# Optimization experiments

Measured on AMD Instinct MI355X. Metric: run time of the kernel, lower is better.

## Reference

```python
import jax, jax.numpy as jnp
import numpy as np

B, N_LR, N_HR, D, NH, L, K = 16, 256, 512, 512, 8, 4, 4
FF = 4 * D

def _ln(x, g, b):
    m = jnp.mean(x, -1, keepdims=True)
    v = jnp.var(x, -1, keepdims=True)
    return (x - m) * jax.lax.rsqrt(v + 1e-5) * g + b

def _gelu(x):
    return jax.nn.gelu(x, approximate=False)  # torch nn.GELU default = exact

def _attn(x, qkvW, qkvb, projW, projb, bias):
    b, n, d = x.shape
    hd = d // NH
    qkv = (x @ qkvW + qkvb).reshape(b, n, 3, NH, hd).transpose(2, 0, 3, 1, 4)
    q, k, v = qkv[0], qkv[1], qkv[2]
    a = jnp.einsum('bhnd,bhmd->bhnm', q, k) * (hd ** -0.5)
    if bias is not None:
        a = a + bias
    a = jax.nn.softmax(a, axis=-1)
    o = jnp.einsum('bhnm,bhmd->bhnd', a, v).transpose(0, 2, 1, 3).reshape(b, n, d)
    return o @ projW + projb

def _ffn(x, W1, b1, W2, b2):
    return _gelu(x @ W1 + b1) @ W2 + b2

def setup_inputs() -> dict:
    key = jax.random.key(0)
    ks = iter(jax.random.split(key, 64))
    def rn(shape, s=0.02):
        return jax.random.normal(next(ks), shape, jnp.float32) * s
    inp = {}
    A = rn((B, N_LR, N_LR), 1.0)
    A = 0.5 * (A + A.transpose(0, 2, 1))  # symmetric weighted adjacency
    inp['A_lr'] = A
    inp['X_lr'] = A  # node features = adjacency rows, as in the original model
    inp['ip_W'] = rn((N_LR, D)); inp['ip_b'] = jnp.zeros(D)
    inp['ip_g'] = jnp.ones(D); inp['ip_bt'] = jnp.zeros(D)
    inp['e_n1g'] = jnp.ones((L, D)); inp['e_n1b'] = jnp.zeros((L, D))
    inp['e_qkvW'] = rn((L, D, 3 * D)); inp['e_qkvb'] = jnp.zeros((L, 3 * D))
    inp['e_projW'] = rn((L, D, D)); inp['e_projb'] = jnp.zeros((L, D))
    inp['e_ebW'] = rn((L, NH), 1.0); inp['e_ebs'] = jnp.full((L,), 0.1)
    inp['e_n2g'] = jnp.ones((L, D)); inp['e_n2b'] = jnp.zeros((L, D))
    inp['e_f1W'] = rn((L, D, FF)); inp['e_f1b'] = jnp.zeros((L, FF))
    inp['e_f2W'] = rn((L, FF, D)); inp['e_f2b'] = jnp.zeros((L, D))
    inp['encn_g'] = jnp.ones(D); inp['encn_b'] = jnp.zeros(D)
    inp['up1W'] = rn((N_LR, N_HR)); inp['up1b'] = jnp.zeros(N_HR)
    inp['up2W'] = rn((N_HR, N_HR)); inp['up2b'] = jnp.zeros(N_HR)
    inp['r_n1g'] = jnp.ones(D); inp['r_n1b'] = jnp.zeros(D)
    inp['r_qkvW'] = rn((D, 3 * D)); inp['r_qkvb'] = jnp.zeros(3 * D)
    inp['r_projW'] = rn((D, D)); inp['r_projb'] = jnp.zeros(D)
    inp['r_n2g'] = jnp.ones(D); inp['r_n2b'] = jnp.zeros(D)
    inp['r_f1W'] = rn((D, FF)); inp['r_f1b'] = jnp.zeros(FF)
    inp['r_f2W'] = rn((FF, D)); inp['r_f2b'] = jnp.zeros(D)
    inp['hrn_g'] = jnp.ones(D); inp['hrn_b'] = jnp.zeros(D)
    inp['dec_W'] = rn((K, D, D)); inp['dec_b'] = jnp.full((1,), 3.0)
    return inp

def reference(A_lr, X_lr, ip_W, ip_b, ip_g, ip_bt, e_n1g, e_n1b, e_qkvW, e_qkvb, e_projW, e_projb, e_ebW, e_ebs, e_n2g, e_n2b, e_f1W, e_f1b, e_f2W, e_f2b, encn_g, encn_b, up1W, up1b, up2W, up2b, r_n1g, r_n1b, r_qkvW, r_qkvb, r_projW, r_projb, r_n2g, r_n2b, r_f1W, r_f1b, r_f2W, r_f2b, hrn_g, hrn_b, dec_W, dec_b):
    # input_proj: Linear -> LayerNorm -> GELU (dropout is identity in eval)
    H = _gelu(_ln(X_lr @ ip_W + ip_b, ip_g, ip_bt))  # (B, n_lr, D)
    # encoder: pre-norm blocks with additive per-head edge bias in softmax
    for l in range(L):
        bias = e_ebs[l] * A_lr[:, None, :, :] * e_ebW[l][None, :, None, None]  # (B,NH,N,N)
        H = H + _attn(_ln(H, e_n1g[l], e_n1b[l]), e_qkvW[l], e_qkvb[l], e_projW[l], e_projb[l], bias)
        H = H + _ffn(_ln(H, e_n2g[l], e_n2b[l]), e_f1W[l], e_f1b[l], e_f2W[l], e_f2b[l])
    H = _ln(H, encn_g, encn_b)
    # upsample n_lr -> n_hr along node axis (applied on transposed H)
    Ht = H.transpose(0, 2, 1)                      # (B, D, n_lr)
    Ht = _gelu(Ht @ up1W + up1b) @ up2W + up2b     # (B, D, n_hr)
    H = Ht.transpose(0, 2, 1)                      # (B, n_hr, D)
    # HR refinement: standard pre-norm self-attention block
    H = H + _attn(_ln(H, r_n1g, r_n1b), r_qkvW, r_qkvb, r_projW, r_projb, None)
    H = H + _ffn(_ln(H, r_n2g, r_n2b), r_f1W, r_f1b, r_f2W, r_f2b)
    H = _ln(H, hrn_g, hrn_b)
    # bilinear multi-head decoder: mean_k H W_k H^T, symmetrized
    A_pred = jnp.einsum('bnd,kde,bme->bnm', H, dec_W, H) / K
    A_pred = 0.5 * (A_pred + A_pred.transpose(0, 2, 1))
    iu, ju = np.triu_indices(N_HR, k=1)
    pred = A_pred[:, iu, ju]                        # (B, n_hr*(n_hr-1)/2)
    return jax.nn.softplus(pred + dec_b[0])
```

## Files before the change

### kernel.cpp

```cpp
#include <hip/hip_runtime.h>
#include <hip/hip_bf16.h>
#include <math.h>

#define DEV __device__ __forceinline__

typedef __attribute__((ext_vector_type(8))) short bf16x8;
typedef __attribute__((ext_vector_type(4))) float f32x4;

DEV float gelu_f(float x) { return 0.5f * x * (1.0f + erff(x * 0.70710678118654752f)); }

DEV float block_reduce(float v, bool is_sum, float* red) {
#pragma unroll
  for (int off = 32; off > 0; off >>= 1) {
    float o = __shfl_down(v, off, 64);
    v = is_sum ? (v + o) : fmaxf(v, o);
  }
  __syncthreads();
  if ((threadIdx.x & 63) == 0) red[threadIdx.x >> 6] = v;
  __syncthreads();
  return is_sum ? (red[0] + red[1] + red[2] + red[3])
                : fmaxf(fmaxf(red[0], red[1]), fmaxf(red[2], red[3]));
}

DEV short bf16s(float x) {
  __hip_bfloat16 v = __float2bfloat16(x);
  return *reinterpret_cast<short*>(&v);
}

DEV void async16(void* lds, const void* g) {
  __builtin_amdgcn_global_load_lds(
      (const __attribute__((address_space(1))) unsigned int*)g,
      (__attribute__((address_space(3))) unsigned int*)lds, 16, 0, 0);
}

__global__ __launch_bounds__(256) void conv_kernel(
    const float* __restrict__ X, __hip_bfloat16* __restrict__ Y, int n) {
  int i = blockIdx.x * 256 + threadIdx.x;
  if (i < n) Y[i] = __float2bfloat16(X[i]);
}

__global__ __launch_bounds__(256) void tconv_kernel(
    const float* __restrict__ X, __hip_bfloat16* __restrict__ Y, int R, int C) {
  __shared__ float t[32][33];
  const float* xb = X + (size_t)blockIdx.z * R * C;
  __hip_bfloat16* yb = Y + (size_t)blockIdx.z * R * C;
  int c0 = blockIdx.x * 32, r0 = blockIdx.y * 32;
  int tx = threadIdx.x & 31, ty = threadIdx.x >> 5;
  for (int i = ty; i < 32; i += 8) t[i][tx] = xb[(size_t)(r0 + i) * C + c0 + tx];
  __syncthreads();
  for (int i = ty; i < 32; i += 8)
    yb[(size_t)(c0 + i) * R + r0 + tx] = __float2bfloat16(t[tx][i]);
}

__global__ __launch_bounds__(256) void build_s_kernel(
    const float* __restrict__ W, __hip_bfloat16* __restrict__ S, int D, int Kk) {
  int i = blockIdx.x * 256 + threadIdx.x;
  if (i >= D * D) return;
  int d = i / D, e = i % D;
  float s = 0.f;
  for (int k = 0; k < Kk; ++k) {
    s += W[(size_t)k * D * D + i];
    s += W[(size_t)k * D * D + (size_t)e * D + d];
  }
  S[i] = __float2bfloat16(s / (2.0f * Kk));
}

__global__ __launch_bounds__(256) void mgemm_kernel(
    const __hip_bfloat16* __restrict__ A, const __hip_bfloat16* __restrict__ Bt,
    const float* __restrict__ bias, const float* __restrict__ resid,
    float* __restrict__ outf, __hip_bfloat16* __restrict__ outb,
    int M, int N, int K, int act, int mgrp) {
  __shared__ __align__(16) short As[64 * 64];
  __shared__ __align__(16) short Bs[64 * 64];
  const int tid = threadIdx.x;
  const int lane = tid & 63, wave = tid >> 6;
  const int quad = lane >> 4, l15 = lane & 15;
  const int bid = blockIdx.x;
  const int g = bid & 7, sidx = bid >> 3;
  const int mt = g * mgrp + sidx % mgrp;
  const int nt = sidx / mgrp;
  const int row0 = mt * 64, col0 = nt * 64;
  const short* Ag = (const short*)A;
  const short* Bg = (const short*)Bt;
  f32x4 acc[4] = {};

  for (int k0 = 0; k0 < K; k0 += 64) {
    __syncthreads();
#pragma unroll
    for (int i = 0; i < 2; ++i) {
      int c = (wave * 2 + i) * 64 + lane;
      int r = c >> 3, pp = c & 7;
      int kc = pp ^ (r & 7);
      async16(&As[(wave * 2 + i) * 512], &Ag[(size_t)(row0 + r) * K + k0 + kc * 8]);
      async16(&Bs[(wave * 2 + i) * 512], &Bg[(size_t)(col0 + r) * K + k0 + kc * 8]);
    }
    __syncthreads();
#pragma unroll
    for (int kh = 0; kh < 2; ++kh) {
      const int ch = ((quad + kh * 4) ^ (l15 & 7)) * 8;
      bf16x8 af = *(const bf16x8*)&As[(wave * 16 + l15) * 64 + ch];
#pragma unroll
      for (int ni = 0; ni < 4; ++ni) {
        bf16x8 bq = *(const bf16x8*)&Bs[(ni * 16 + l15) * 64 + ch];
        acc[ni] = __builtin_amdgcn_mfma_f32_16x16x32_bf16(af, bq, acc[ni], 0, 0, 0);
      }
    }
  }

#pragma unroll
  for (int ni = 0; ni < 4; ++ni) {
    int cc = col0 + ni * 16 + l15;
    float bb = bias ? bias[cc] : 0.f;
#pragma unroll
    for (int r = 0; r < 4; ++r) {
      int rr = row0 + wave * 16 + quad * 4 + r;
      size_t idx = (size_t)rr * N + cc;
      float v = acc[ni][r] + bb;
      if (act) v = gelu_f(v);
      if (resid) v += resid[idx];
      if (outf) outf[idx] = v;
      if (outb) outb[idx] = __float2bfloat16(v);
    }
  }
}

__global__ __launch_bounds__(256) void qkv_gemm_kernel(
    const __hip_bfloat16* __restrict__ A, const __hip_bfloat16* __restrict__ Bt,
    const float* __restrict__ bias, __hip_bfloat16* __restrict__ qkv,
    int M, int K, int nseq, int lgn, int mgrp) {
  __shared__ __align__(16) short As[64 * 64];
  __shared__ __align__(16) short Bs[64 * 64];
  const int tid = threadIdx.x;
  const int lane = tid & 63, wave = tid >> 6;
  const int quad = lane >> 4, l15 = lane & 15;
  const int bid = blockIdx.x;
  const int g = bid & 7, sidx = bid >> 3;
  const int mt = g * mgrp + sidx % mgrp;
  const int nt = sidx / mgrp;
  const int row0 = mt * 64, col0 = nt * 64;
  const short* Ag = (const short*)A;
  const short* Bg = (const short*)Bt;
  f32x4 acc[4] = {};

  for (int k0 = 0; k0 < K; k0 += 64) {
    __syncthreads();
#pragma unroll
    for (int i = 0; i < 2; ++i) {
      int c = (wave * 2 + i) * 64 + lane;
      int r = c >> 3, pp = c & 7;
      int kc = pp ^ (r & 7);
      async16(&As[(wave * 2 + i) * 512], &Ag[(size_t)(row0 + r) * K + k0 + kc * 8]);
      async16(&Bs[(wave * 2 + i) * 512], &Bg[(size_t)(col0 + r) * K + k0 + kc * 8]);
    }
    __syncthreads();
#pragma unroll
    for (int kh = 0; kh < 2; ++kh) {
      const int ch = ((quad + kh * 4) ^ (l15 & 7)) * 8;
      bf16x8 af = *(const bf16x8*)&As[(wave * 16 + l15) * 64 + ch];
#pragma unroll
      for (int ni = 0; ni < 4; ++ni) {
        bf16x8 bq = *(const bf16x8*)&Bs[(ni * 16 + l15) * 64 + ch];
        acc[ni] = __builtin_amdgcn_mfma_f32_16x16x32_bf16(af, bq, acc[ni], 0, 0, 0);
      }
    }
  }

  const size_t PART = (size_t)M * 512;
#pragma unroll
  for (int ni = 0; ni < 4; ++ni) {
    int cc = col0 + ni * 16 + l15;
    float bb = bias ? bias[cc] : 0.f;
    int which = cc >> 9;
    int h = (cc >> 6) & 7;
    int d = cc & 63;
#pragma unroll
    for (int r = 0; r < 4; ++r) {
      int rr = row0 + wave * 16 + quad * 4 + r;
      int b = rr >> lgn;
      int nn = rr & (nseq - 1);
      float v = acc[ni][r] + bb;
      size_t dst;
      if (which == 2) {
        dst = 2 * PART + (((size_t)b * 8 + h) * 64 + d) * nseq + nn;
      } else {
        dst = (size_t)which * PART + (((size_t)b * 8 + h) * nseq + nn) * 64 + d;
      }
      qkv[dst] = __float2bfloat16(v);
    }
  }
}

__global__ __launch_bounds__(256) void fattn_kernel(
    const __hip_bfloat16* __restrict__ Qh, const __hip_bfloat16* __restrict__ Kh,
    const __hip_bfloat16* __restrict__ Vt, __hip_bfloat16* __restrict__ O,
    const float* __restrict__ Abias, const float* __restrict__ ebW,
    const float* __restrict__ ebs, int N) {
  __shared__ __align__(16) short Ks[64][72];
  __shared__ __align__(16) short Vs[64][72];
  __shared__ __align__(16) short Ps[4][16][72];
  const int qt = blockIdx.x, h = blockIdx.y, b = blockIdx.z;
  const int tid = threadIdx.x, lane = tid & 63, wave = tid >> 6;
  const int quad = lane >> 4, l15 = lane & 15;
  const size_t hb = (size_t)b * 8 + h;
  const short* Qg = (const short*)Qh + hb * N * 64;
  const short* Kg = (const short*)Kh + hb * N * 64;
  const short* Vg = (const short*)Vt + hb * 64 * N;
  const float scale = 0.125f;
  const bool hasb = (Abias != nullptr);
  const float bscale = hasb ? ebs[0] * ebW[h] : 0.f;
  const int qrow_w = qt * 64 + wave * 16;

  bf16x8 qf0 = *(const bf16x8*)&Qg[(size_t)(qrow_w + l15) * 64 + quad * 8];
  bf16x8 qf1 = *(const bf16x8*)&Qg[(size_t)(qrow_w + l15) * 64 + quad * 8 + 32];

  float m_i[4], l_i[4];
  f32x4 oacc[4] = {};
#pragma unroll
  for (int r = 0; r < 4; ++r) { m_i[r] = -1e30f; l_i[r] = 0.f; }

  for (int k0 = 0; k0 < N; k0 += 64) {
    __syncthreads();
#pragma unroll
    for (int i = 0; i < 2; ++i) {
      int idx = i * 256 + tid;
      int r = idx >> 3, ch = idx & 7;
      *(uint4*)&Ks[r][ch * 8] = *(const uint4*)&Kg[(size_t)(k0 + r) * 64 + ch * 8];
      *(uint4*)&Vs[r][ch * 8] = *(const uint4*)&Vg[(size_t)r * N + k0 + ch * 8];
    }
    __syncthreads();

    f32x4 s[4] = {};
#pragma unroll
    for (int ni = 0; ni < 4; ++ni) {
      bf16x8 kf0 = *(const bf16x8*)&Ks[ni * 16 + l15][quad * 8];
      bf16x8 kf1 = *(const bf16x8*)&Ks[ni * 16 + l15][quad * 8 + 32];
      s[ni] = __builtin_amdgcn_mfma_f32_16x16x32_bf16(qf0, kf0, s[ni], 0, 0, 0);
      s[ni] = __builtin_amdgcn_mfma_f32_16x16x32_bf16(qf1, kf1, s[ni], 0, 0, 0);
    }
    if (hasb) {
#pragma unroll
      for (int ni = 0; ni < 4; ++ni)
#pragma unroll
        for (int r = 0; r < 4; ++r) {
          int qq = qrow_w + quad * 4 + r;
          int kk = k0 + ni * 16 + l15;
          s[ni][r] = s[ni][r] * scale + bscale * Abias[((size_t)b * N + qq) * N + kk];
        }
    } else {
#pragma unroll
      for (int ni = 0; ni < 4; ++ni)
#pragma unroll
        for (int r = 0; r < 4; ++r) s[ni][r] *= scale;
    }

    float mt[4];
#pragma unroll
    for (int r = 0; r < 4; ++r)
      mt[r] = fmaxf(fmaxf(s[0][r], s[1][r]), fmaxf(s[2][r], s[3][r]));
#pragma unroll
    for (int off = 1; off < 16; off <<= 1)
#pragma unroll
      for (int r = 0; r < 4; ++r) mt[r] = fmaxf(mt[r], __shfl_xor(mt[r], off, 64));

    float alpha[4];
#pragma unroll
    for (int r = 0; r < 4; ++r) {
      float mn = fmaxf(m_i[r], mt[r]);
      alpha[r] = __expf(m_i[r] - mn);
      m_i[r] = mn;
    }
    float ls[4] = {0.f, 0.f, 0.f, 0.f};
#pragma unroll
    for (int ni = 0; ni < 4; ++ni)
#pragma unroll
      for (int r = 0; r < 4; ++r) {
        float p = __expf(s[ni][r] - m_i[r]);
        s[ni][r] = p;
        ls[r] += p;
      }
#pragma unroll
    for (int off = 1; off < 16; off <<= 1)
#pragma unroll
      for (int r = 0; r < 4; ++r) ls[r] += __shfl_xor(ls[r], off, 64);
#pragma unroll
    for (int r = 0; r < 4; ++r) l_i[r] = l_i[r] * alpha[r] + ls[r];
#pragma unroll
    for (int ni = 0; ni < 4; ++ni)
#pragma unroll
      for (int r = 0; r < 4; ++r) oacc[ni][r] *= alpha[r];

#pragma unroll
    for (int ni = 0; ni < 4; ++ni)
#pragma unroll
      for (int r = 0; r < 4; ++r)
        Ps[wave][quad * 4 + r][ni * 16 + l15] = bf16s(s[ni][r]);

    bf16x8 pf0 = *(const bf16x8*)&Ps[wave][l15][quad * 8];
    bf16x8 pf1 = *(const bf16x8*)&Ps[wave][l15][quad * 8 + 32];
#pragma unroll
    for (int ni = 0; ni < 4; ++ni) {
      bf16x8 vf0 = *(const bf16x8*)&Vs[ni * 16 + l15][quad * 8];
      bf16x8 vf1 = *(const bf16x8*)&Vs[ni * 16 + l15][quad * 8 + 32];
      oacc[ni] = __builtin_amdgcn_mfma_f32_16x16x32_bf16(pf0, vf0, oacc[ni], 0, 0, 0);
      oacc[ni] = __builtin_amdgcn_mfma_f32_16x16x32_bf16(pf1, vf1, oacc[ni], 0, 0, 0);
    }
  }

  float inv[4];
#pragma unroll
  for (int r = 0; r < 4; ++r) inv[r] = 1.f / l_i[r];
#pragma unroll
  for (int ni = 0; ni < 4; ++ni)
#pragma unroll
    for (int r = 0; r < 4; ++r) {
      int nn = qrow_w + quad * 4 + r;
      int col = h * 64 + ni * 16 + l15;
      O[((size_t)b * N + nn) * 512 + col] = __float2bfloat16(oacc[ni][r] * inv[r]);
    }
}

__global__ __launch_bounds__(256) void dec_mfma_kernel(
    const __hip_bfloat16* __restrict__ Tb_, const __hip_bfloat16* __restrict__ Hb_,
    const float* __restrict__ dec_b, float* __restrict__ out) {
  const int Nn = 512, K = 512;
  __shared__ __align__(16) short As[64 * 64];
  __shared__ __align__(16) short Bs[64 * 64];
  int p = blockIdx.x;
  int bb = blockIdx.y;
  int it = 0, rem = p;
  while (rem >= 8 - it) { rem -= 8 - it; ++it; }
  int jt = it + rem;
  const int row0 = it * 64, col0 = jt * 64;
  const int tid = threadIdx.x;
  const int lane = tid & 63, wave = tid >> 6;
  const int quad = lane >> 4, l15 = lane & 15;
  const int wr = (wave >> 1) * 32, wc = (wave & 1) * 32;
  const short* Ag = (const short*)(Tb_ + (size_t)bb * Nn * K);
  const short* Bg = (const short*)(Hb_ + (size_t)bb * Nn * K);
  f32x4 acc[2][2] = {};

  for (int k0 = 0; k0 < K; k0 += 64) {
    __syncthreads();
#pragma unroll
    for (int i = 0; i < 2; ++i) {
      int c = (wave * 2 + i) * 64 + lane;
      int r = c >> 3, pp = c & 7;
      int kc = pp ^ (r & 7);
      async16(&As[(wave * 2 + i) * 512], &Ag[(size_t)(row0 + r) * K + k0 + kc * 8]);
      async16(&Bs[(wave * 2 + i) * 512], &Bg[(size_t)(col0 + r) * K + k0 + kc * 8]);
    }
    __syncthreads();
#pragma unroll
    for (int kh = 0; kh < 2; ++kh) {
      const int ch = ((quad + kh * 4) ^ (l15 & 7)) * 8;
      bf16x8 af[2], bq[2];
#pragma unroll
      for (int mi = 0; mi < 2; ++mi)
        af[mi] = *(const bf16x8*)&As[(wr + mi * 16 + l15) * 64 + ch];
#pragma unroll
      for (int ni = 0; ni < 2; ++ni)
        bq[ni] = *(const bf16x8*)&Bs[(wc + ni * 16 + l15) * 64 + ch];
#pragma unroll
      for (int mi = 0; mi < 2; ++mi)
#pragma unroll
        for (int ni = 0; ni < 2; ++ni)
          acc[mi][ni] = __builtin_amdgcn_mfma_f32_16x16x32_bf16(af[mi], bq[ni], acc[mi][ni], 0, 0, 0);
    }
  }

  float db = dec_b[0];
  size_t obase = (size_t)bb * ((size_t)Nn * (Nn - 1) / 2);
#pragma unroll
  for (int mi = 0; mi < 2; ++mi) {
#pragma unroll
    for (int ni = 0; ni < 2; ++ni) {
      int j = col0 + wc + ni * 16 + l15;
#pragma unroll
      for (int r = 0; r < 4; ++r) {
        int i = row0 + wr + mi * 16 + quad * 4 + r;
        if (j > i) {
          float x = acc[mi][ni][r] + db;
          float sp = fmaxf(x, 0.f) + __logf(1.f + __expf(-fabsf(x)));
          out[obase + (size_t)i * (2 * Nn - i - 1) / 2 + (j - i - 1)] = sp;
        }
      }
    }
  }
}

__global__ __launch_bounds__(256) void ln_kernel(
    const float* __restrict__ X, float* __restrict__ outf,
    __hip_bfloat16* __restrict__ outb, const float* __restrict__ g,
    const float* __restrict__ b, int D, int do_gelu) {
  __shared__ float red[4];
  int row = blockIdx.x;
  const float* x = X + (size_t)row * D;
  float s = 0.f, s2 = 0.f;
  for (int d = threadIdx.x; d < D; d += 256) {
    float v = x[d];
    s += v;
    s2 += v * v;
  }
  s = block_reduce(s, true, red);
  s2 = block_reduce(s2, true, red);
  float mean = s / D;
  float var = s2 / D - mean * mean;
  float inv = rsqrtf(var + 1e-5f);
  for (int d = threadIdx.x; d < D; d += 256) {
    float v = (x[d] - mean) * inv * g[d] + b[d];
    if (do_gelu) v = gelu_f(v);
    if (outf) outf[(size_t)row * D + d] = v;
    if (outb) outb[(size_t)row * D + d] = __float2bfloat16(v);
  }
}

template <typename T>
__global__ __launch_bounds__(256) void transpose_kernel(
    const T* __restrict__ X, T* __restrict__ Y, int R, int C) {
  __shared__ T t[32][33];
  const T* xb = X + (size_t)blockIdx.z * R * C;
  T* yb = Y + (size_t)blockIdx.z * R * C;
  int c0 = blockIdx.x * 32, r0 = blockIdx.y * 32;
  int tx = threadIdx.x & 31, ty = threadIdx.x >> 5;
  for (int i = ty; i < 32; i += 8) t[i][tx] = xb[(size_t)(r0 + i) * C + c0 + tx];
  __syncthreads();
  for (int i = ty; i < 32; i += 8) yb[(size_t)(c0 + i) * R + r0 + tx] = t[tx][i];
}

extern "C" void kernel_launch(void* const* d_in, const int* in_sizes, int n_in,
                              void* d_out, int out_size, void* d_ws, size_t ws_size,
                              hipStream_t stream) {
  const float *A_lr = (const float*)d_in[0], *X_lr = (const float*)d_in[1],
              *ip_W = (const float*)d_in[2], *ip_b = (const float*)d_in[3],
              *ip_g = (const float*)d_in[4], *ip_bt = (const float*)d_in[5],
              *e_n1g = (const float*)d_in[6], *e_n1b = (const float*)d_in[7],
              *e_qkvW = (const float*)d_in[8], *e_qkvb = (const float*)d_in[9],
              *e_projW = (const float*)d_in[10], *e_projb = (const float*)d_in[11],
              *e_ebW = (const float*)d_in[12], *e_ebs = (const float*)d_in[13],
              *e_n2g = (const float*)d_in[14], *e_n2b = (const float*)d_in[15],
              *e_f1W = (const float*)d_in[16], *e_f1b = (const float*)d_in[17],
              *e_f2W = (const float*)d_in[18], *e_f2b = (const float*)d_in[19],
              *encn_g = (const float*)d_in[20], *encn_b = (const float*)d_in[21],
              *up1W = (const float*)d_in[22], *up1b = (const float*)d_in[23],
              *up2W = (const float*)d_in[24], *up2b = (const float*)d_in[25],
              *r_n1g = (const float*)d_in[26], *r_n1b = (const float*)d_in[27],
              *r_qkvW = (const float*)d_in[28], *r_qkvb = (const float*)d_in[29],
              *r_projW = (const float*)d_in[30], *r_projb = (const float*)d_in[31],
              *r_n2g = (const float*)d_in[32], *r_n2b = (const float*)d_in[33],
              *r_f1W = (const float*)d_in[34], *r_f1b = (const float*)d_in[35],
              *r_f2W = (const float*)d_in[36], *r_f2b = (const float*)d_in[37],
              *hrn_g = (const float*)d_in[38], *hrn_b = (const float*)d_in[39],
              *dec_W = (const float*)d_in[40], *dec_b = (const float*)d_in[41];

  const int Bb = 16, NLR = 256, NHR = 512, Dm = 512, NHh = 8, FF = 2048, Ll = 4;
  typedef __hip_bfloat16 bf;

  float* ws = (float*)d_ws;
  float* H = ws;
  float* Hf = ws + 4194304;
  bf* XNb = (bf*)(ws + 8388608);
  bf* AOb = (bf*)(ws + 10485760);
  bf* BIGb = (bf*)(ws + 12582912);
  bf* WB = (bf*)(ws + 20971520);
  bf* Xlrb = (bf*)(ws + 29229056);

  size_t o = 0;
  bf* ipWt = WB + o;   o += (size_t)512 * 256;
  bf* eqkvT = WB + o;  o += (size_t)4 * 1536 * 512;
  bf* eprojT = WB + o; o += (size_t)4 * 512 * 512;
  bf* ef1T = WB + o;   o += (size_t)4 * 2048 * 512;
  bf* ef2T = WB + o;   o += (size_t)4 * 512 * 2048;
  bf* up1T = WB + o;   o += (size_t)512 * 256;
  bf* up2T = WB + o;   o += (size_t)512 * 512;
  bf* rqkvT = WB + o;  o += (size_t)1536 * 512;
  bf* rprojT = WB + o; o += (size_t)512 * 512;
  bf* rf1T = WB + o;   o += (size_t)2048 * 512;
  bf* rf2T = WB + o;   o += (size_t)512 * 2048;
  bf* Sb = WB + o;     o += (size_t)512 * 512;

  bf* Q_e = BIGb;
  bf* K_e = BIGb + 2097152;
  bf* V_e = BIGb + 4194304;
  bf* Q_r = BIGb;
  bf* K_r = BIGb + 4194304;
  bf* V_r = BIGb + 8388608;

  tconv_kernel<<<dim3(16, 8, 1), 256, 0, stream>>>(ip_W, ipWt, 256, 512);
  tconv_kernel<<<dim3(48, 16, 4), 256, 0, stream>>>(e_qkvW, eqkvT, 512, 1536);
  tconv_kernel<<<dim3(16, 16, 4), 256, 0, stream>>>(e_projW, eprojT, 512, 512);
  tconv_kernel<<<dim3(64, 16, 4), 256, 0, stream>>>(e_f1W, ef1T, 512, 2048);
  tconv_kernel<<<dim3(16, 64, 4), 256, 0, stream>>>(e_f2W, ef2T, 2048, 512);
  tconv_kernel<<<dim3(16, 8, 1), 256, 0, stream>>>(up1W, up1T, 256, 512);
  tconv_kernel<<<dim3(16, 16, 1), 256, 0, stream>>>(up2W, up2T, 512, 512);
  tconv_kernel<<<dim3(48, 16, 1), 256, 0, stream>>>(r_qkvW, rqkvT, 512, 1536);
  tconv_kernel<<<dim3(16, 16, 1), 256, 0, stream>>>(r_projW, rprojT, 512, 512);
  tconv_kernel<<<dim3(64, 16, 1), 256, 0, stream>>>(r_f1W, rf1T, 512, 2048);
  tconv_kernel<<<dim3(16, 64, 1), 256, 0, stream>>>(r_f2W, rf2T, 2048, 512);
  conv_kernel<<<(1048576 + 255) / 256, 256, 0, stream>>>(X_lr, Xlrb, 1048576);
  build_s_kernel<<<(512 * 512 + 255) / 256, 256, 0, stream>>>(dec_W, Sb, Dm, 4);

  mgemm_kernel<<<64 * 8, 256, 0, stream>>>(
      Xlrb, ipWt, ip_b, nullptr, Hf, nullptr, Bb * NLR, Dm, NLR, 0, 8);
  ln_kernel<<<Bb * NLR, 256, 0, stream>>>(Hf, H, nullptr, ip_g, ip_bt, Dm, 1);

  for (int l = 0; l < Ll; ++l) {
    ln_kernel<<<Bb * NLR, 256, 0, stream>>>(H, nullptr, XNb, e_n1g + l * Dm, e_n1b + l * Dm, Dm, 0);
    qkv_gemm_kernel<<<64 * 24, 256, 0, stream>>>(
        XNb, eqkvT + (size_t)l * 1536 * 512, e_qkvb + l * 1536, BIGb,
        Bb * NLR, Dm, NLR, 8, 8);
    fattn_kernel<<<dim3(4, 8, 16), 256, 0, stream>>>(
        Q_e, K_e, V_e, AOb, A_lr, e_ebW + l * NHh, e_ebs + l, NLR);
    mgemm_kernel<<<64 * 8, 256, 0, stream>>>(
        AOb, eprojT + (size_t)l * 512 * 512, e_projb + l * Dm, H,
        H, nullptr, Bb * NLR, Dm, Dm, 0, 8);
    ln_kernel<<<Bb * NLR, 256, 0, stream>>>(H, nullptr, XNb, e_n2g + l * Dm, e_n2b + l * Dm, Dm, 0);
    mgemm_kernel<<<64 * 32, 256, 0, stream>>>(
        XNb, ef1T + (size_t)l * 2048 * 512, e_f1b + l * FF, nullptr,
        nullptr, BIGb, Bb * NLR, FF, Dm, 1, 8);
    mgemm_kernel<<<64 * 8, 256, 0, stream>>>(
        BIGb, ef2T + (size_t)l * 512 * 2048, e_f2b + l * Dm, H,
        H, nullptr, Bb * NLR, Dm, FF, 0, 8);
  }

  ln_kernel<<<Bb * NLR, 256, 0, stream>>>(H, nullptr, XNb, encn_g, encn_b, Dm, 0);
  transpose_kernel<bf><<<dim3(16, 8, Bb), 256, 0, stream>>>(XNb, AOb, NLR, Dm);
  mgemm_kernel<<<128 * 8, 256, 0, stream>>>(
      AOb, up1T, up1b, nullptr, nullptr, BIGb, Bb * Dm, NHR, NLR, 1, 16);
  mgemm_kernel<<<128 * 8, 256, 0, stream>>>(
      BIGb, up2T, up2b, nullptr, Hf, nullptr, Bb * Dm, NHR, NHR, 0, 16);
  transpose_kernel<float><<<dim3(16, 16, Bb), 256, 0, stream>>>(Hf, H, Dm, NHR);

  ln_kernel<<<Bb * NHR, 256, 0, stream>>>(H, nullptr, XNb, r_n1g, r_n1b, Dm, 0);
  qkv_gemm_kernel<<<128 * 24, 256, 0, stream>>>(
      XNb, rqkvT, r_qkvb, BIGb, Bb * NHR, Dm, NHR, 9, 16);
  fattn_kernel<<<dim3(8, 8, 16), 256, 0, stream>>>(
      Q_r, K_r, V_r, AOb, nullptr, nullptr, nullptr, NHR);
  mgemm_kernel<<<128 * 8, 256, 0, stream>>>(
      AOb, rprojT, r_projb, H, H, nullptr, Bb * NHR, Dm, Dm, 0, 16);
  ln_kernel<<<Bb * NHR, 256, 0, stream>>>(H, nullptr, XNb, r_n2g, r_n2b, Dm, 0);
  mgemm_kernel<<<128 * 32, 256, 0, stream>>>(
      XNb, rf1T, r_f1b, nullptr, nullptr, BIGb, Bb * NHR, FF, Dm, 1, 16);
  mgemm_kernel<<<128 * 8, 256, 0, stream>>>(
      BIGb, rf2T, r_f2b, H, H, nullptr, Bb * NHR, Dm, FF, 0, 16);

  ln_kernel<<<Bb * NHR, 256, 0, stream>>>(H, nullptr, XNb, hrn_g, hrn_b, Dm, 0);
  mgemm_kernel<<<128 * 8, 256, 0, stream>>>(
      XNb, Sb, nullptr, nullptr, nullptr, AOb, Bb * NHR, Dm, Dm, 0, 16);
  dec_mfma_kernel<<<dim3(36, Bb), 256, 0, stream>>>(
      AOb, XNb, dec_b, (float*)d_out);
}
```

Baseline: 911.4 us.

## Store adjacency bias as bf16 and remap attention blocks for XCD locality

The adjacency bias used in encoder attention is converted once to bf16 after the input projection, reusing the Xlrb buffer, and the attention kernel reads bf16 bias instead of fp32. This halves the bias bytes read per layer. The attention grid is also flattened to 1D with a swizzle so each XCD (bid&7) handles a pair of batches, aiming for better L2 reuse of K/V and bias. Reusing Xlrb is safe only if nothing reads the old bf16 X_lr after the input GEMM, and bf16 bias adds slight rounding error.

```diff
diff --git a/kernel.cpp b/kernel.cpp
--- a/kernel.cpp
+++ b/kernel.cpp
@@ -193,12 +193,18 @@
 __global__ __launch_bounds__(256) void fattn_kernel(
     const __hip_bfloat16* __restrict__ Qh, const __hip_bfloat16* __restrict__ Kh,
     const __hip_bfloat16* __restrict__ Vt, __hip_bfloat16* __restrict__ O,
-    const float* __restrict__ Abias, const float* __restrict__ ebW,
-    const float* __restrict__ ebs, int N) {
+    const __hip_bfloat16* __restrict__ Abias, const float* __restrict__ ebW,
+    const float* __restrict__ ebs, int N, int lgq) {
   __shared__ __align__(16) short Ks[64][72];
   __shared__ __align__(16) short Vs[64][72];
   __shared__ __align__(16) short Ps[4][16][72];
-  const int qt = blockIdx.x, h = blockIdx.y, b = blockIdx.z;
+  const int bid = blockIdx.x;
+  const int g = bid & 7, s = bid >> 3;
+  const int bloc = s >> (lgq + 3);
+  const int rem = s & ((8 << lgq) - 1);
+  const int h = rem >> lgq;
+  const int qt = rem & ((1 << lgq) - 1);
+  const int b = g * 2 + bloc;
   const int tid = threadIdx.x, lane = tid & 63, wave = tid >> 6;
   const int quad = lane >> 4, l15 = lane & 15;
   const size_t hb = (size_t)b * 8 + h;
@@ -229,13 +235,13 @@
     }
     __syncthreads();
 
-    f32x4 s[4] = {};
+    f32x4 sv[4] = {};
 #pragma unroll
     for (int ni = 0; ni < 4; ++ni) {
       bf16x8 kf0 = *(const bf16x8*)&Ks[ni * 16 + l15][quad * 8];
       bf16x8 kf1 = *(const bf16x8*)&Ks[ni * 16 + l15][quad * 8 + 32];
-      s[ni] = __builtin_amdgcn_mfma_f32_16x16x32_bf16(qf0, kf0, s[ni], 0, 0, 0);
-      s[ni] = __builtin_amdgcn_mfma_f32_16x16x32_bf16(qf1, kf1, s[ni], 0, 0, 0);
+      sv[ni] = __builtin_amdgcn_mfma_f32_16x16x32_bf16(qf0, kf0, sv[ni], 0, 0, 0);
+      sv[ni] = __builtin_amdgcn_mfma_f32_16x16x32_bf16(qf1, kf1, sv[ni], 0, 0, 0);
     }
     if (hasb) {
 #pragma unroll
@@ -244,19 +250,20 @@
         for (int r = 0; r < 4; ++r) {
           int qq = qrow_w + quad * 4 + r;
           int kk = k0 + ni * 16 + l15;
-          s[ni][r] = s[ni][r] * scale + bscale * Abias[((size_t)b * N + qq) * N + kk];
+          float ab = __bfloat162float(Abias[((size_t)b * N + qq) * N + kk]);
+          sv[ni][r] = sv[ni][r] * scale + bscale * ab;
         }
     } else {
 #pragma unroll
       for (int ni = 0; ni < 4; ++ni)
 #pragma unroll
-        for (int r = 0; r < 4; ++r) s[ni][r] *= scale;
+        for (int r = 0; r < 4; ++r) sv[ni][r] *= scale;
     }
 
     float mt[4];
 #pragma unroll
     for (int r = 0; r < 4; ++r)
-      mt[r] = fmaxf(fmaxf(s[0][r], s[1][r]), fmaxf(s[2][r], s[3][r]));
+      mt[r] = fmaxf(fmaxf(sv[0][r], sv[1][r]), fmaxf(sv[2][r], sv[3][r]));
 #pragma unroll
     for (int off = 1; off < 16; off <<= 1)
 #pragma unroll
@@ -274,8 +281,8 @@
     for (int ni = 0; ni < 4; ++ni)
 #pragma unroll
       for (int r = 0; r < 4; ++r) {
-        float p = __expf(s[ni][r] - m_i[r]);
-        s[ni][r] = p;
+        float p = __expf(sv[ni][r] - m_i[r]);
+        sv[ni][r] = p;
         ls[r] += p;
       }
 #pragma unroll
@@ -293,7 +300,7 @@
     for (int ni = 0; ni < 4; ++ni)
 #pragma unroll
       for (int r = 0; r < 4; ++r)
-        Ps[wave][quad * 4 + r][ni * 16 + l15] = bf16s(s[ni][r]);
+        Ps[wave][quad * 4 + r][ni * 16 + l15] = bf16s(sv[ni][r]);
 
     bf16x8 pf0 = *(const bf16x8*)&Ps[wave][l15][quad * 8];
     bf16x8 pf1 = *(const bf16x8*)&Ps[wave][l15][quad * 8 + 32];
@@ -484,6 +491,7 @@
   bf* Q_r = BIGb;
   bf* K_r = BIGb + 4194304;
   bf* V_r = BIGb + 8388608;
+  bf* Albrb = Xlrb;
 
   tconv_kernel<<<dim3(16, 8, 1), 256, 0, stream>>>(ip_W, ipWt, 256, 512);
   tconv_kernel<<<dim3(48, 16, 4), 256, 0, stream>>>(e_qkvW, eqkvT, 512, 1536);
@@ -502,14 +510,15 @@
   mgemm_kernel<<<64 * 8, 256, 0, stream>>>(
       Xlrb, ipWt, ip_b, nullptr, Hf, nullptr, Bb * NLR, Dm, NLR, 0, 8);
   ln_kernel<<<Bb * NLR, 256, 0, stream>>>(Hf, H, nullptr, ip_g, ip_bt, Dm, 1);
+  conv_kernel<<<(1048576 + 255) / 256, 256, 0, stream>>>(A_lr, Albrb, 1048576);
 
   for (int l = 0; l < Ll; ++l) {
     ln_kernel<<<Bb * NLR, 256, 0, stream>>>(H, nullptr, XNb, e_n1g + l * Dm, e_n1b + l * Dm, Dm, 0);
     qkv_gemm_kernel<<<64 * 24, 256, 0, stream>>>(
         XNb, eqkvT + (size_t)l * 1536 * 512, e_qkvb + l * 1536, BIGb,
         Bb * NLR, Dm, NLR, 8, 8);
-    fattn_kernel<<<dim3(4, 8, 16), 256, 0, stream>>>(
-        Q_e, K_e, V_e, AOb, A_lr, e_ebW + l * NHh, e_ebs + l, NLR);
+    fattn_kernel<<<16 * 8 * 4, 256, 0, stream>>>(
+        Q_e, K_e, V_e, AOb, Albrb, e_ebW + l * NHh, e_ebs + l, NLR, 2);
     mgemm_kernel<<<64 * 8, 256, 0, stream>>>(
         AOb, eprojT + (size_t)l * 512 * 512, e_projb + l * Dm, H,
         H, nullptr, Bb * NLR, Dm, Dm, 0, 8);
@@ -533,8 +542,8 @@
   ln_kernel<<<Bb * NHR, 256, 0, stream>>>(H, nullptr, XNb, r_n1g, r_n1b, Dm, 0);
   qkv_gemm_kernel<<<128 * 24, 256, 0, stream>>>(
       XNb, rqkvT, r_qkvb, BIGb, Bb * NHR, Dm, NHR, 9, 16);
-  fattn_kernel<<<dim3(8, 8, 16), 256, 0, stream>>>(
-      Q_r, K_r, V_r, AOb, nullptr, nullptr, nullptr, NHR);
+  fattn_kernel<<<16 * 8 * 8, 256, 0, stream>>>(
+      Q_r, K_r, V_r, AOb, nullptr, nullptr, nullptr, NHR, 3);
   mgemm_kernel<<<128 * 8, 256, 0, stream>>>(
       AOb, rprojT, r_projb, H, H, nullptr, Bb * NHR, Dm, Dm, 0, 16);
   ln_kernel<<<Bb * NHR, 256, 0, stream>>>(H, nullptr, XNb, r_n2g, r_n2b, Dm, 0);
```

New measurement: 911.1 us. About the same (-0.0%).
